# Performance work log

Hardware: AMD Instinct MI355X
Metric: run time of the kernel (lower is better)

Reference implementation:

```python
import jax, jax.numpy as jnp
import numpy as np

B, T, D, K = 8, 2048, 384, 64

def setup_inputs() -> dict:
    key = jax.random.key(0)
    k1, k2, k3, k4 = jax.random.split(key, 4)
    x = jax.random.normal(k1, (B, T, D), dtype=jnp.float32)
    # torch nn.Linear default init scale ~ 1/sqrt(fan_in); use scaled normals
    Wq = jax.random.normal(k2, (D, K), dtype=jnp.float32) / np.sqrt(D)
    Wk = jax.random.normal(k3, (D, K), dtype=jnp.float32) / np.sqrt(D)
    Wv = jax.random.normal(k4, (D, D), dtype=jnp.float32) / np.sqrt(D)
    return {"x": x, "Wq": Wq, "Wk": Wk, "Wv": Wv}

def reference(x, Wq, Wk, Wv):
    # x: (B,T,D)
    q = jnp.einsum('btd,dk->btk', x, Wq)      # (B,T,K)
    k = jnp.einsum('btd,dk->btk', x, Wk)      # (B,T,K)
    v = jnp.einsum('btd,de->bte', x, Wv)      # (B,T,D)
    scores = jnp.einsum('bqk,bsk->bqs', q, k) / jnp.sqrt(jnp.float32(K))  # (B,T,T)
    causal = jnp.tril(jnp.ones((T, T), dtype=bool))
    scores = jnp.where(causal, scores, -jnp.inf)
    weights = jax.nn.softmax(scores, axis=-1)
    out = jnp.einsum('bqs,bse->bqe', weights, v)  # (B,T,D)
    return out
```

## Files before the change

kernel.cpp:

```cpp
#include <hip/hip_runtime.h>

#define TT 2048
#define DD 384

typedef float f32x4 __attribute__((ext_vector_type(4)));
typedef float f32x16 __attribute__((ext_vector_type(16)));
typedef short s16x8 __attribute__((ext_vector_type(8)));
typedef short s16x2 __attribute__((ext_vector_type(2)));
typedef unsigned int u32x4 __attribute__((ext_vector_type(4)));

typedef __attribute__((address_space(3))) unsigned char* as3p;
typedef const __attribute__((address_space(1))) unsigned char* as1p;
#define GLLDS(gsrc, ldst) __builtin_amdgcn_global_load_lds((as1p)(gsrc), (as3p)(ldst), 16, 0, 0)

static __device__ __forceinline__ unsigned short f2bf(float f) {
    unsigned int u = __builtin_bit_cast(unsigned int, f);
    u = (u + 0x7fffu + ((u >> 16) & 1u)) >> 16;
    return (unsigned short)u;
}
static __device__ __forceinline__ unsigned int pk2(float a, float b) {
#if __has_builtin(__builtin_amdgcn_cvt_pk_bf16_f32)
    s16x2 t = __builtin_amdgcn_cvt_pk_bf16_f32(a, b);
    return __builtin_bit_cast(unsigned int, t);
#else
    unsigned int ua = __builtin_bit_cast(unsigned int, a);
    unsigned int ub = __builtin_bit_cast(unsigned int, b);
    ua = (ua + 0x7fffu + ((ua >> 16) & 1u)) >> 16;
    ub = (ub + 0x7fffu + ((ub >> 16) & 1u)) & 0xffff0000u;
    return ua | ub;
#endif
}

__global__ __launch_bounds__(256, 2) void qkv_gemm(
    const float* __restrict__ x, const float* __restrict__ Wq,
    const float* __restrict__ Wk, const float* __restrict__ Wv,
    unsigned short* __restrict__ qo, unsigned short* __restrict__ ko,
    unsigned short* __restrict__ vto)
{
    __shared__ __align__(16) unsigned short lds[16384];
    const int tid = threadIdx.x;
    const int l   = tid & 63;
    const int w   = tid >> 6;
    const int si  = l & 15;
    const int qq  = l >> 4;
    const int m0  = blockIdx.x * 128;
    const int nb  = blockIdx.y;
    const int wr  = w >> 1, wc = w & 1;

    const int bn = tid & 127;
    const int bk = (tid >> 7) * 16;
    const float* wsrc; int ldw;
    if (nb == 0) { wsrc = (bn < 64) ? (Wq + bn) : (Wk + (bn - 64)); ldw = 64; }
    else         { wsrc = Wv + (nb - 1) * 128 + bn;                 ldw = 384; }

    f32x4 acc[4][4];
    #pragma unroll
    for (int rt = 0; rt < 4; ++rt)
        #pragma unroll
        for (int ct = 0; ct < 4; ++ct) acc[rt][ct] = (f32x4){0.f, 0.f, 0.f, 0.f};

    for (int kt = 0; kt < 12; ++kt) {
        const int k0 = kt * 32;
        #pragma unroll
        for (int i = 0; i < 2; ++i) {
            const int u = tid + 256 * i, r = u >> 2, c = u & 3;
            const float* xp = x + (size_t)(m0 + r) * DD + k0 + c * 8;
            f32x4 x0 = *(const f32x4*)xp;
            f32x4 x1 = *(const f32x4*)(xp + 4);
            s16x8 av;
            av[0] = (short)f2bf(x0[0]); av[1] = (short)f2bf(x0[1]);
            av[2] = (short)f2bf(x0[2]); av[3] = (short)f2bf(x0[3]);
            av[4] = (short)f2bf(x1[0]); av[5] = (short)f2bf(x1[1]);
            av[6] = (short)f2bf(x1[2]); av[7] = (short)f2bf(x1[3]);
            *(s16x8*)&lds[r * 32 + ((c ^ (r & 3)) * 8)] = av;
        }
        {
            float t[16];
            #pragma unroll
            for (int j = 0; j < 16; ++j) t[j] = wsrc[(size_t)(k0 + bk + j) * ldw];
            #pragma unroll
            for (int jj = 0; jj < 2; ++jj) {
                s16x8 bv;
                #pragma unroll
                for (int j = 0; j < 8; ++j) bv[j] = (short)f2bf(t[jj * 8 + j]);
                const int ch = (tid >> 7) * 2 + jj;
                *(s16x8*)&lds[4096 + bn * 32 + ((ch ^ (bn & 3)) * 8)] = bv;
            }
        }
        __syncthreads();

        s16x8 af[4], bf[4];
        #pragma unroll
        for (int rt = 0; rt < 4; ++rt) {
            const int row = wr * 64 + rt * 16 + si;
            af[rt] = *(const s16x8*)&lds[row * 32 + ((qq ^ (row & 3)) * 8)];
        }
        #pragma unroll
        for (int ct = 0; ct < 4; ++ct) {
            const int col = wc * 64 + ct * 16 + si;
            bf[ct] = *(const s16x8*)&lds[4096 + col * 32 + ((qq ^ (col & 3)) * 8)];
        }
        #pragma unroll
        for (int rt = 0; rt < 4; ++rt)
            #pragma unroll
            for (int ct = 0; ct < 4; ++ct)
                acc[rt][ct] = __builtin_amdgcn_mfma_f32_16x16x32_bf16(af[rt], bf[ct], acc[rt][ct], 0, 0, 0);
        __syncthreads();
    }

    if (nb == 0) {
        if (wc == 0) {
            #pragma unroll
            for (int rt = 0; rt < 4; ++rt)
                #pragma unroll
                for (int ct = 0; ct < 4; ++ct)
                    #pragma unroll
                    for (int r = 0; r < 4; ++r) {
                        const int m = m0 + wr * 64 + rt * 16 + qq * 4 + r;
                        qo[(size_t)m * 64 + ct * 16 + si] = f2bf(acc[rt][ct][r] * 0.125f);
                    }
        } else {
            #pragma unroll
            for (int rt = 0; rt < 4; ++rt)
                #pragma unroll
                for (int ct = 0; ct < 4; ++ct)
                    #pragma unroll
                    for (int r = 0; r < 4; ++r) {
                        const int m = m0 + wr * 64 + rt * 16 + qq * 4 + r;
                        const int col = ct * 16 + si;
                        ko[(size_t)m * 64 + (((col >> 3) ^ (m & 7)) * 8) + (col & 7)] = f2bf(acc[rt][ct][r]);
                    }
        }
    } else {
        #pragma unroll
        for (int rt = 0; rt < 4; ++rt)
            #pragma unroll
            for (int ct = 0; ct < 4; ++ct)
                #pragma unroll
                for (int r = 0; r < 4; ++r) {
                    const int m = wr * 64 + rt * 16 + qq * 4 + r;
                    const int n = wc * 64 + ct * 16 + si;
                    lds[n * 128 + (((m >> 3) ^ (n & 7)) * 8) + (m & 7)] = f2bf(acc[rt][ct][r]);
                }
        __syncthreads();
        const int bbat = m0 >> 11, t0 = m0 & 2047;
        #pragma unroll
        for (int i = 0; i < 8; ++i) {
            const int u = tid + 256 * i, n = u >> 4, mc = u & 15;
            s16x8 v = *(const s16x8*)&lds[n * 128 + ((mc ^ (n & 7)) * 8)];
            *(s16x8*)&vto[((size_t)bbat * DD + ((nb - 1) * 128 + n)) * TT
                          + t0 + (mc >> 3) * 64 + (((mc & 7) ^ (n & 7)) * 8)] = v;
        }
    }
}

__global__ __launch_bounds__(1024, 4) void attn(
    const unsigned short* __restrict__ qg, const unsigned short* __restrict__ kg,
    const unsigned short* __restrict__ vg, float* __restrict__ out)
{
    __shared__ __align__(16) unsigned short lds[40960];

    const int tid = threadIdx.x;
    const int l   = tid & 63;
    const int w   = tid >> 6;
    const int q4  = w >> 2;
    const int qb  = w & 3;
    const int lo  = l & 31;
    const int hi  = l >> 5;
    const int h   = q4 >> 1;
    const int ct  = q4 & 1;

    const int g  = blockIdx.x;
    const int bb = g & 7;
    const int eq = (g >> 3) & 3;
    const int j  = 15 - (g >> 5);
    const int q0 = j * 128;
    const int e0 = eq * 96;
    const int qrow = q0 + qb * 32 + lo;

    s16x8 qf[4];
    {
        const unsigned short* qp = qg + ((size_t)bb * TT + qrow) * 64;
        #pragma unroll
        for (int st = 0; st < 4; ++st) qf[st] = *(const s16x8*)(qp + st * 16 + hi * 8);
    }

    f32x16 o[3];
    #pragma unroll
    for (int et = 0; et < 3; ++et)
        #pragma unroll
        for (int r = 0; r < 16; ++r) o[et][r] = 0.f;
    float lp = 0.f;

    const unsigned short* kbase = kg + (size_t)bb * TT * 64;
    const unsigned short* vbase = vg + ((size_t)bb * DD + e0) * TT;

    const unsigned short* kS = kbase + w * 512 + l * 8;
    const int chA = w,      pA = chA / 12, rrA = (chA % 12) * 8;
    const int chB = 16 + w, pB = chB / 12, rrB = (chB % 12) * 8;
    const unsigned short* vSA = vbase + ((size_t)(rrA + (l >> 3))) * TT + pA * 64 + (l & 7) * 8;
    const unsigned short* vSB = vbase + ((size_t)(rrB + (l >> 3))) * TT + pB * 64 + (l & 7) * 8;

    #define STAGE(IT, BUF)                                                   \
    {                                                                        \
        unsigned short* kl = &lds[(BUF) * 8192];                             \
        GLLDS(kS + (size_t)(IT) * 8192, &kl[w * 512]);                       \
        unsigned short* vl = &lds[16384 + (BUF) * 12288];                    \
        GLLDS(vSA + (IT) * 128, &vl[chA * 512]);                             \
        if (w < 8) GLLDS(vSB + (IT) * 128, &vl[chB * 512]);                  \
    }

    STAGE(0, 0);

    for (int it = 0; it <= j; ++it) {
        const int buf = it & 1;
        __syncthreads();

        if (it < j) STAGE(it + 1, 1 - buf);

        const unsigned short* Ks = &lds[buf * 8192 + h * 4096];
        const unsigned short* Vs = &lds[16384 + buf * 12288 + h * 6144];

        const int sq = it * 128 + q4 * 32;
        if (sq <= q0 + qb * 32 + 31) {
            const bool mb = (sq + 31 > q0 + qb * 32);
            f32x16 sa;
            #pragma unroll
            for (int r = 0; r < 16; ++r) sa[r] = 0.f;
            #pragma unroll
            for (int st = 0; st < 4; ++st) {
                s16x8 kf = *(const s16x8*)&Ks[(ct * 32 + lo) * 64 + (((st * 2 + hi) ^ (lo & 7)) * 8)];
                sa = __builtin_amdgcn_mfma_f32_32x32x16_bf16(kf, qf[st], sa, 0, 0, 0);
            }
            float pv[16];
            #pragma unroll
            for (int r = 0; r < 16; ++r) {
                float e = __expf(sa[r]);
                if (mb) {
                    const int srow = sq + (r & 3) + 8 * (r >> 2) + 4 * hi;
                    if (srow > qrow) e = 0.f;
                }
                pv[r] = e;
                lp += e;
            }
            unsigned int d0 = pk2(pv[0], pv[1]),   d1 = pk2(pv[2], pv[3]);
            unsigned int d2 = pk2(pv[4], pv[5]),   d3 = pk2(pv[6], pv[7]);
            unsigned int d4 = pk2(pv[8], pv[9]),   d5 = pk2(pv[10], pv[11]);
            unsigned int d6 = pk2(pv[12], pv[13]), d7 = pk2(pv[14], pv[15]);
            unsigned int sA0 = hi ? d0 : d2, sA1 = hi ? d1 : d3;
            unsigned int rA0 = (unsigned int)__shfl_xor((int)sA0, 32);
            unsigned int rA1 = (unsigned int)__shfl_xor((int)sA1, 32);
            u32x4 fa0 = hi ? (u32x4){rA0, rA1, d2, d3} : (u32x4){d0, d1, rA0, rA1};
            unsigned int sB0 = hi ? d4 : d6, sB1 = hi ? d5 : d7;
            unsigned int rB0 = (unsigned int)__shfl_xor((int)sB0, 32);
            unsigned int rB1 = (unsigned int)__shfl_xor((int)sB1, 32);
            u32x4 fa1 = hi ? (u32x4){rB0, rB1, d6, d7} : (u32x4){d4, d5, rB0, rB1};
            s16x8 a0 = __builtin_bit_cast(s16x8, fa0);
            s16x8 a1 = __builtin_bit_cast(s16x8, fa1);
            #pragma unroll
            for (int et = 0; et < 3; ++et) {
                const int el = et * 32 + lo;
                s16x8 v0 = *(const s16x8*)&Vs[el * 64 + (((ct * 4 + hi) ^ (el & 7)) * 8)];
                o[et] = __builtin_amdgcn_mfma_f32_32x32x16_bf16(a0, v0, o[et], 0, 0, 0);
                s16x8 v1 = *(const s16x8*)&Vs[el * 64 + (((ct * 4 + 2 + hi) ^ (el & 7)) * 8)];
                o[et] = __builtin_amdgcn_mfma_f32_32x32x16_bf16(a1, v1, o[et], 0, 0, 0);
            }
        }
    }
    __syncthreads();

    float* stL = (float*)lds;
    float* fb  = (float*)lds + 512;
    lp += __shfl_xor(lp, 32);
    if (hi == 0) stL[q4 * 128 + qb * 32 + lo] = lp;
    __syncthreads();

    #pragma unroll
    for (int ph = 0; ph < 2; ++ph) {
        if (q4 != 0 && (qb >> 1) == ph) {
            const int slot = (q4 - 1) * 64 + (qb & 1) * 32;
            #pragma unroll
            for (int r = 0; r < 16; ++r) {
                const int rloc = (r & 3) + 8 * (r >> 2) + 4 * hi;
                #pragma unroll
                for (int et = 0; et < 3; ++et)
                    fb[(slot + rloc) * 96 + et * 32 + lo] = o[et][r];
            }
        }
        __syncthreads();
        if (q4 == 0 && (qb >> 1) == ph) {
            const int slot = (qb & 1) * 32;
            #pragma unroll
            for (int r = 0; r < 16; ++r) {
                const int rloc = (r & 3) + 8 * (r >> 2) + 4 * hi;
                const int rr = qb * 32 + rloc;
                const float linv = 1.f / (stL[rr] + stL[128 + rr] + stL[256 + rr] + stL[384 + rr]);
                float* op = out + ((size_t)bb * TT + q0 + rr) * DD + e0;
                #pragma unroll
                for (int et = 0; et < 3; ++et)
                    op[et * 32 + lo] = (o[et][r]
                        + fb[(0 * 64 + slot + rloc) * 96 + et * 32 + lo]
                        + fb[(1 * 64 + slot + rloc) * 96 + et * 32 + lo]
                        + fb[(2 * 64 + slot + rloc) * 96 + et * 32 + lo]) * linv;
            }
        }
        __syncthreads();
    }
    #undef STAGE
}

extern "C" void kernel_launch(void* const* d_in, const int* in_sizes, int n_in,
                              void* d_out, int out_size, void* d_ws, size_t ws_size,
                              hipStream_t stream)
{
    const float* x  = (const float*)d_in[0];
    const float* Wq = (const float*)d_in[1];
    const float* Wk = (const float*)d_in[2];
    const float* Wv = (const float*)d_in[3];

    unsigned short* qws  = (unsigned short*)d_ws;
    unsigned short* kws  = (unsigned short*)((char*)d_ws + ((size_t)2 << 20));
    unsigned short* vtws = (unsigned short*)((char*)d_ws + ((size_t)4 << 20));

    qkv_gemm<<<dim3(128, 4), dim3(256), 0, stream>>>(x, Wq, Wk, Wv, qws, kws, vtws);
    attn<<<dim3(512), dim3(1024), 0, stream>>>(qws, kws, vtws, (float*)d_out);
}
```

Baseline: 150.4 us.

## Split fused attention into separate QK/softmax and PV kernels via materialized P

```diff
diff --git a/kernel.cpp b/kernel.cpp
--- a/kernel.cpp
+++ b/kernel.cpp
@@ -154,30 +154,29 @@
     }
 }
 
-__global__ __launch_bounds__(1024, 4) void attn(
+__global__ __launch_bounds__(256, 4) void qk_pass(
     const unsigned short* __restrict__ qg, const unsigned short* __restrict__ kg,
-    const unsigned short* __restrict__ vg, float* __restrict__ out)
+    unsigned short* __restrict__ Pws, float* __restrict__ lpart)
 {
-    __shared__ __align__(16) unsigned short lds[40960];
-
+    __shared__ __align__(16) unsigned short kl[8192];
     const int tid = threadIdx.x;
     const int l   = tid & 63;
     const int w   = tid >> 6;
-    const int q4  = w >> 2;
-    const int qb  = w & 3;
     const int lo  = l & 31;
     const int hi  = l >> 5;
-    const int h   = q4 >> 1;
-    const int ct  = q4 & 1;
-
-    const int g  = blockIdx.x;
-    const int bb = g & 7;
-    const int eq = (g >> 3) & 3;
-    const int j  = 15 - (g >> 5);
-    const int q0 = j * 128;
-    const int e0 = eq * 96;
-    const int qrow = q0 + qb * 32 + lo;
-
+    const int t   = blockIdx.x;
+    const int bb  = blockIdx.y;
+
+    int j = 0, acc = 0;
+    while (acc + j + 1 <= t) { acc += j + 1; ++j; }
+    const int it = t - acc;
+
+    const unsigned short* kS = kg + (size_t)bb * TT * 64 + (size_t)it * 8192;
+    #pragma unroll
+    for (int c = 0; c < 4; ++c)
+        GLLDS(kS + (w * 4 + c) * 512 + l * 8, &kl[(w * 4 + c) * 512]);
+
+    const int qrow = j * 128 + w * 32 + lo;
     s16x8 qf[4];
     {
         const unsigned short* qp = qg + ((size_t)bb * TT + qrow) * 64;
@@ -185,81 +184,120 @@
         for (int st = 0; st < 4; ++st) qf[st] = *(const s16x8*)(qp + st * 16 + hi * 8);
     }
 
-    f32x16 o[3];
-    #pragma unroll
-    for (int et = 0; et < 3; ++et)
+    __syncthreads();
+
+    float lp = 0.f;
+    const bool onD = (it == j);
+    unsigned short* pt = Pws + (size_t)(bb * 136 + t) * 16384;
+    const int nsq = onD ? (w + 1) : 4;
+    for (int sq = 0; sq < nsq; ++sq) {
+        f32x16 sa;
+        #pragma unroll
+        for (int r = 0; r < 16; ++r) sa[r] = 0.f;
+        #pragma unroll
+        for (int st = 0; st < 4; ++st) {
+            s16x8 kf = *(const s16x8*)&kl[(sq * 32 + lo) * 64 + (((st * 2 + hi) ^ (lo & 7)) * 8)];
+            sa = __builtin_amdgcn_mfma_f32_32x32x16_bf16(kf, qf[st], sa, 0, 0, 0);
+        }
+        const bool mb = onD && (sq == w);
+        float pv[16];
+        #pragma unroll
+        for (int r = 0; r < 16; ++r) {
+            float e = __expf(sa[r]);
+            if (mb) {
+                const int srow = it * 128 + sq * 32 + (r & 3) + 8 * (r >> 2) + 4 * hi;
+                if (srow > qrow) e = 0.f;
+            }
+            pv[r] = e;
+            lp += e;
+        }
+        unsigned int d0 = pk2(pv[0], pv[1]),   d1 = pk2(pv[2], pv[3]);
+        unsigned int d2 = pk2(pv[4], pv[5]),   d3 = pk2(pv[6], pv[7]);
+        unsigned int d4 = pk2(pv[8], pv[9]),   d5 = pk2(pv[10], pv[11]);
+        unsigned int d6 = pk2(pv[12], pv[13]), d7 = pk2(pv[14], pv[15]);
+        unsigned int sA0 = hi ? d0 : d2, sA1 = hi ? d1 : d3;
+        unsigned int rA0 = (unsigned int)__shfl_xor((int)sA0, 32);
+        unsigned int rA1 = (unsigned int)__shfl_xor((int)sA1, 32);
+        u32x4 fa0 = hi ? (u32x4){rA0, rA1, d2, d3} : (u32x4){d0, d1, rA0, rA1};
+        unsigned int sB0 = hi ? d4 : d6, sB1 = hi ? d5 : d7;
+        unsigned int rB0 = (unsigned int)__shfl_xor((int)sB0, 32);
+        unsigned int rB1 = (unsigned int)__shfl_xor((int)sB1, 32);
+        u32x4 fa1 = hi ? (u32x4){rB0, rB1, d6, d7} : (u32x4){d4, d5, rB0, rB1};
+        *(s16x8*)(pt + (w * 4 + sq) * 1024 + l * 8)       = __builtin_bit_cast(s16x8, fa0);
+        *(s16x8*)(pt + (w * 4 + sq) * 1024 + 512 + l * 8) = __builtin_bit_cast(s16x8, fa1);
+    }
+    lp += __shfl_xor(lp, 32);
+    if (hi == 0)
+        lpart[((size_t)bb * 16 + it) * 2048 + (size_t)j * 128 + w * 32 + lo] = lp;
+}
+
+__global__ __launch_bounds__(512, 4) void pv_pass(
+    const unsigned short* __restrict__ Pws, const unsigned short* __restrict__ vg,
+    const float* __restrict__ lpart, float* __restrict__ out)
+{
+    __shared__ __align__(16) unsigned short vl[32768];
+    __shared__ float linv[128];
+    const int tid = threadIdx.x;
+    const int l   = tid & 63;
+    const int w   = tid >> 6;
+    const int qb  = w >> 1;
+    const int ew  = w & 1;
+    const int lo  = l & 31;
+    const int hi  = l >> 5;
+
+    const int g  = blockIdx.x;
+    const int m  = g >> 1, p = g & 1;
+    const int jj = m / 12;
+    const int j  = p ? jj : 15 - jj;
+    const int combo = (m % 12) * 2 + p;
+    const int bb = combo & 7;
+    const int eb = combo >> 3;
+
+    const unsigned short* ptile = Pws + (size_t)(bb * 136 + j * (j + 1) / 2) * 16384;
+    const unsigned short* vbase = vg + ((size_t)bb * DD + eb * 128) * TT;
+
+    if (tid < 128) {
+        float s = 0.f;
+        for (int it = 0; it <= j; ++it)
+            s += lpart[((size_t)bb * 16 + it) * 2048 + (size_t)j * 128 + tid];
+        linv[tid] = 1.f / s;
+    }
+
+    const unsigned short* vS[4];
+    #pragma unroll
+    for (int c = 0; c < 4; ++c) {
+        const int ch = w * 4 + c, ph = ch >> 4, rg = ch & 15;
+        vS[c] = vbase + (size_t)(rg * 8 + (l >> 3)) * TT + ph * 64 + (l & 7) * 8;
+    }
+    #define VSTAGE(IT, BUF)                                                     \
+    {                                                                           \
+        _Pragma("unroll")                                                       \
+        for (int c = 0; c < 4; ++c)                                             \
+            GLLDS(vS[c] + (size_t)(IT) * 128, &vl[(BUF) * 16384 + (w * 4 + c) * 512]); \
+    }
+
+    f32x16 o[2];
+    #pragma unroll
+    for (int et = 0; et < 2; ++et)
         #pragma unroll
         for (int r = 0; r < 16; ++r) o[et][r] = 0.f;
-    float lp = 0.f;
-
-    const unsigned short* kbase = kg + (size_t)bb * TT * 64;
-    const unsigned short* vbase = vg + ((size_t)bb * DD + e0) * TT;
-
-    const unsigned short* kS = kbase + w * 512 + l * 8;
-    const int chA = w,      pA = chA / 12, rrA = (chA % 12) * 8;
-    const int chB = 16 + w, pB = chB / 12, rrB = (chB % 12) * 8;
-    const unsigned short* vSA = vbase + ((size_t)(rrA + (l >> 3))) * TT + pA * 64 + (l & 7) * 8;
-    const unsigned short* vSB = vbase + ((size_t)(rrB + (l >> 3))) * TT + pB * 64 + (l & 7) * 8;
-
-    #define STAGE(IT, BUF)                                                   \
-    {                                                                        \
-        unsigned short* kl = &lds[(BUF) * 8192];                             \
-        GLLDS(kS + (size_t)(IT) * 8192, &kl[w * 512]);                       \
-        unsigned short* vl = &lds[16384 + (BUF) * 12288];                    \
-        GLLDS(vSA + (IT) * 128, &vl[chA * 512]);                             \
-        if (w < 8) GLLDS(vSB + (IT) * 128, &vl[chB * 512]);                  \
-    }
-
-    STAGE(0, 0);
-
+
+    VSTAGE(0, 0);
     for (int it = 0; it <= j; ++it) {
         const int buf = it & 1;
         __syncthreads();
-
-        if (it < j) STAGE(it + 1, 1 - buf);
-
-        const unsigned short* Ks = &lds[buf * 8192 + h * 4096];
-        const unsigned short* Vs = &lds[16384 + buf * 12288 + h * 6144];
-
-        const int sq = it * 128 + q4 * 32;
-        if (sq <= q0 + qb * 32 + 31) {
-            const bool mb = (sq + 31 > q0 + qb * 32);
-            f32x16 sa;
-            #pragma unroll
-            for (int r = 0; r < 16; ++r) sa[r] = 0.f;
-            #pragma unroll
-            for (int st = 0; st < 4; ++st) {
-                s16x8 kf = *(const s16x8*)&Ks[(ct * 32 + lo) * 64 + (((st * 2 + hi) ^ (lo & 7)) * 8)];
-                sa = __builtin_amdgcn_mfma_f32_32x32x16_bf16(kf, qf[st], sa, 0, 0, 0);
-            }
-            float pv[16];
-            #pragma unroll
-            for (int r = 0; r < 16; ++r) {
-                float e = __expf(sa[r]);
-                if (mb) {
-                    const int srow = sq + (r & 3) + 8 * (r >> 2) + 4 * hi;
-                    if (srow > qrow) e = 0.f;
-                }
-                pv[r] = e;
-                lp += e;
-            }
-            unsigned int d0 = pk2(pv[0], pv[1]),   d1 = pk2(pv[2], pv[3]);
-            unsigned int d2 = pk2(pv[4], pv[5]),   d3 = pk2(pv[6], pv[7]);
-            unsigned int d4 = pk2(pv[8], pv[9]),   d5 = pk2(pv[10], pv[11]);
-            unsigned int d6 = pk2(pv[12], pv[13]), d7 = pk2(pv[14], pv[15]);
-            unsigned int sA0 = hi ? d0 : d2, sA1 = hi ? d1 : d3;
-            unsigned int rA0 = (unsigned int)__shfl_xor((int)sA0, 32);
-            unsigned int rA1 = (unsigned int)__shfl_xor((int)sA1, 32);
-            u32x4 fa0 = hi ? (u32x4){rA0, rA1, d2, d3} : (u32x4){d0, d1, rA0, rA1};
-            unsigned int sB0 = hi ? d4 : d6, sB1 = hi ? d5 : d7;
-            unsigned int rB0 = (unsigned int)__shfl_xor((int)sB0, 32);
-            unsigned int rB1 = (unsigned int)__shfl_xor((int)sB1, 32);
-            u32x4 fa1 = hi ? (u32x4){rB0, rB1, d6, d7} : (u32x4){d4, d5, rB0, rB1};
-            s16x8 a0 = __builtin_bit_cast(s16x8, fa0);
-            s16x8 a1 = __builtin_bit_cast(s16x8, fa1);
-            #pragma unroll
-            for (int et = 0; et < 3; ++et) {
-                const int el = et * 32 + lo;
+        if (it < j) VSTAGE(it + 1, 1 - buf);
+
+        const unsigned short* pfr = ptile + (size_t)it * 16384 + qb * 4096;
+        const int nsq = (it == j) ? (qb + 1) : 4;
+        for (int sq = 0; sq < nsq; ++sq) {
+            s16x8 a0 = *(const s16x8*)(pfr + sq * 1024 + l * 8);
+            s16x8 a1 = *(const s16x8*)(pfr + sq * 1024 + 512 + l * 8);
+            const int h = sq >> 1, ct = sq & 1;
+            const unsigned short* Vs = &vl[buf * 16384 + h * 8192];
+            #pragma unroll
+            for (int et = 0; et < 2; ++et) {
+                const int el = ew * 64 + et * 32 + lo;
                 s16x8 v0 = *(const s16x8*)&Vs[el * 64 + (((ct * 4 + hi) ^ (el & 7)) * 8)];
                 o[et] = __builtin_amdgcn_mfma_f32_32x32x16_bf16(a0, v0, o[et], 0, 0, 0);
                 s16x8 v1 = *(const s16x8*)&Vs[el * 64 + (((ct * 4 + 2 + hi) ^ (el & 7)) * 8)];
@@ -267,46 +305,17 @@
             }
         }
     }
-    __syncthreads();
-
-    float* stL = (float*)lds;
-    float* fb  = (float*)lds + 512;
-    lp += __shfl_xor(lp, 32);
-    if (hi == 0) stL[q4 * 128 + qb * 32 + lo] = lp;
-    __syncthreads();
-
-    #pragma unroll
-    for (int ph = 0; ph < 2; ++ph) {
-        if (q4 != 0 && (qb >> 1) == ph) {
-            const int slot = (q4 - 1) * 64 + (qb & 1) * 32;
-            #pragma unroll
-            for (int r = 0; r < 16; ++r) {
-                const int rloc = (r & 3) + 8 * (r >> 2) + 4 * hi;
-                #pragma unroll
-                for (int et = 0; et < 3; ++et)
-                    fb[(slot + rloc) * 96 + et * 32 + lo] = o[et][r];
-            }
-        }
-        __syncthreads();
-        if (q4 == 0 && (qb >> 1) == ph) {
-            const int slot = (qb & 1) * 32;
-            #pragma unroll
-            for (int r = 0; r < 16; ++r) {
-                const int rloc = (r & 3) + 8 * (r >> 2) + 4 * hi;
-                const int rr = qb * 32 + rloc;
-                const float linv = 1.f / (stL[rr] + stL[128 + rr] + stL[256 + rr] + stL[384 + rr]);
-                float* op = out + ((size_t)bb * TT + q0 + rr) * DD + e0;
-                #pragma unroll
-                for (int et = 0; et < 3; ++et)
-                    op[et * 32 + lo] = (o[et][r]
-                        + fb[(0 * 64 + slot + rloc) * 96 + et * 32 + lo]
-                        + fb[(1 * 64 + slot + rloc) * 96 + et * 32 + lo]
-                        + fb[(2 * 64 + slot + rloc) * 96 + et * 32 + lo]) * linv;
-            }
-        }
-        __syncthreads();
-    }
-    #undef STAGE
+    #undef VSTAGE
+
+    #pragma unroll
+    for (int et = 0; et < 2; ++et)
+        #pragma unroll
+        for (int r = 0; r < 16; ++r) {
+            const int rloc = (r & 3) + 8 * (r >> 2) + 4 * hi;
+            const int row  = qb * 32 + rloc;
+            out[((size_t)bb * TT + j * 128 + row) * DD + eb * 128 + ew * 64 + et * 32 + lo]
+                = o[et][r] * linv[row];
+        }
 }
 
 extern "C" void kernel_launch(void* const* d_in, const int* in_sizes, int n_in,
@@ -321,7 +330,10 @@
     unsigned short* qws  = (unsigned short*)d_ws;
     unsigned short* kws  = (unsigned short*)((char*)d_ws + ((size_t)2 << 20));
     unsigned short* vtws = (unsigned short*)((char*)d_ws + ((size_t)4 << 20));
+    unsigned short* Pws  = (unsigned short*)((char*)d_ws + ((size_t)16 << 20));
+    float*          lpart = (float*)((char*)d_ws + ((size_t)16 << 20) + (size_t)8 * 136 * 32768);
 
     qkv_gemm<<<dim3(128, 4), dim3(256), 0, stream>>>(x, Wq, Wk, Wv, qws, kws, vtws);
-    attn<<<dim3(512), dim3(1024), 0, stream>>>(qws, kws, vtws, (float*)d_out);
-}
+    qk_pass<<<dim3(136, 8), dim3(256), 0, stream>>>(qws, kws, Pws, lpart);
+    pv_pass<<<dim3(384), dim3(512), 0, stream>>>(Pws, vtws, lpart, (float*)d_out);
+}
```

After: 150.2 us. No clear change (-0.1%).

## Restructure attention into smaller blocks with software-pipelined PV via LDS-staged probabilities

Applied to the files above, without the earlier changes.

```diff
diff --git a/kernel.cpp b/kernel.cpp
--- a/kernel.cpp
+++ b/kernel.cpp
@@ -154,7 +154,7 @@
     }
 }
 
-__global__ __launch_bounds__(1024, 4) void attn(
+__global__ __launch_bounds__(256, 2) void attn(
     const unsigned short* __restrict__ qg, const unsigned short* __restrict__ kg,
     const unsigned short* __restrict__ vg, float* __restrict__ out)
 {
@@ -163,20 +163,19 @@
     const int tid = threadIdx.x;
     const int l   = tid & 63;
     const int w   = tid >> 6;
-    const int q4  = w >> 2;
-    const int qb  = w & 3;
+    const int qh  = w >> 1;
+    const int eg  = w & 1;
     const int lo  = l & 31;
     const int hi  = l >> 5;
-    const int h   = q4 >> 1;
-    const int ct  = q4 & 1;
-
-    const int g  = blockIdx.x;
-    const int bb = g & 7;
-    const int eq = (g >> 3) & 3;
-    const int j  = 15 - (g >> 5);
-    const int q0 = j * 128;
-    const int e0 = eq * 96;
-    const int qrow = q0 + qb * 32 + lo;
+
+    const int g    = blockIdx.x;
+    const int bb   = g & 7;
+    const int rest = g >> 3;
+    const int eh   = rest % 3;
+    const int q2   = 31 - rest / 3;
+    const int q0   = q2 * 64;
+    const int e0   = eh * 128;
+    const int qrow = q0 + qh * 32 + lo;
 
     s16x8 qf[4];
     {
@@ -185,9 +184,9 @@
         for (int st = 0; st < 4; ++st) qf[st] = *(const s16x8*)(qp + st * 16 + hi * 8);
     }
 
-    f32x16 o[3];
+    f32x16 o[2];
     #pragma unroll
-    for (int et = 0; et < 3; ++et)
+    for (int et = 0; et < 2; ++et)
         #pragma unroll
         for (int r = 0; r < 16; ++r) o[et][r] = 0.f;
     float lp = 0.f;
@@ -195,49 +194,63 @@
     const unsigned short* kbase = kg + (size_t)bb * TT * 64;
     const unsigned short* vbase = vg + ((size_t)bb * DD + e0) * TT;
 
-    const unsigned short* kS = kbase + w * 512 + l * 8;
-    const int chA = w,      pA = chA / 12, rrA = (chA % 12) * 8;
-    const int chB = 16 + w, pB = chB / 12, rrB = (chB % 12) * 8;
-    const unsigned short* vSA = vbase + ((size_t)(rrA + (l >> 3))) * TT + pA * 64 + (l & 7) * 8;
-    const unsigned short* vSB = vbase + ((size_t)(rrB + (l >> 3))) * TT + pB * 64 + (l & 7) * 8;
-
-    #define STAGE(IT, BUF)                                                   \
-    {                                                                        \
-        unsigned short* kl = &lds[(BUF) * 8192];                             \
-        GLLDS(kS + (size_t)(IT) * 8192, &kl[w * 512]);                       \
-        unsigned short* vl = &lds[16384 + (BUF) * 12288];                    \
-        GLLDS(vSA + (IT) * 128, &vl[chA * 512]);                             \
-        if (w < 8) GLLDS(vSB + (IT) * 128, &vl[chB * 512]);                  \
-    }
-
-    STAGE(0, 0);
-
-    for (int it = 0; it <= j; ++it) {
-        const int buf = it & 1;
+    #define STAGE(IT, KB, VB)                                                              \
+    {                                                                                      \
+        GLLDS(kbase + (size_t)(IT) * 4096 + (2 * w) * 512 + l * 8,                         \
+              &lds[(KB) * 4096 + (2 * w) * 512]);                                          \
+        GLLDS(kbase + (size_t)(IT) * 4096 + (2 * w + 1) * 512 + l * 8,                     \
+              &lds[(KB) * 4096 + (2 * w + 1) * 512]);                                      \
+        _Pragma("unroll")                                                                  \
+        for (int c3 = 0; c3 < 4; ++c3) {                                                   \
+            const int rg = 4 * w + c3;                                                     \
+            GLLDS(vbase + (size_t)(rg * 8 + (l >> 3)) * TT + (IT) * 64 + (l & 7) * 8,      \
+                  &lds[8192 + (VB) * 8192 + rg * 512]);                                    \
+        }                                                                                  \
+    }
+
+    #define PVSTEP(VB, PB)                                                                 \
+    {                                                                                      \
+        _Pragma("unroll")                                                                  \
+        for (int ss = 0; ss < 2; ++ss) {                                                   \
+            s16x8 a0 = *(const s16x8*)&lds[32768 + (PB) * 4096 + (qh * 2 + ss) * 1024 + l * 8];       \
+            s16x8 a1 = *(const s16x8*)&lds[32768 + (PB) * 4096 + (qh * 2 + ss) * 1024 + 512 + l * 8]; \
+            _Pragma("unroll")                                                              \
+            for (int et = 0; et < 2; ++et) {                                               \
+                const int el = eg * 64 + et * 32 + lo;                                     \
+                const int vbse = 8192 + (VB) * 8192 + el * 64;                             \
+                s16x8 v0 = *(const s16x8*)&lds[vbse + (((ss * 4 + hi) ^ (el & 7)) * 8)];   \
+                o[et] = __builtin_amdgcn_mfma_f32_32x32x16_bf16(a0, v0, o[et], 0, 0, 0);   \
+                s16x8 v1 = *(const s16x8*)&lds[vbse + (((ss * 4 + 2 + hi) ^ (el & 7)) * 8)]; \
+                o[et] = __builtin_amdgcn_mfma_f32_32x32x16_bf16(a1, v1, o[et], 0, 0, 0);   \
+            }                                                                              \
+        }                                                                                  \
+    }
+
+    STAGE(0, 0, 0);
+
+    int vi = 0, vn = 1;
+    for (int it = 0; it <= q2; ++it) {
+        const int kb = it & 1;
         __syncthreads();
 
-        if (it < j) STAGE(it + 1, 1 - buf);
-
-        const unsigned short* Ks = &lds[buf * 8192 + h * 4096];
-        const unsigned short* Vs = &lds[16384 + buf * 12288 + h * 6144];
-
-        const int sq = it * 128 + q4 * 32;
-        if (sq <= q0 + qb * 32 + 31) {
-            const bool mb = (sq + 31 > q0 + qb * 32);
+        if (it < q2) STAGE(it + 1, 1 - kb, vn);
+
+        {
             f32x16 sa;
             #pragma unroll
             for (int r = 0; r < 16; ++r) sa[r] = 0.f;
             #pragma unroll
             for (int st = 0; st < 4; ++st) {
-                s16x8 kf = *(const s16x8*)&Ks[(ct * 32 + lo) * 64 + (((st * 2 + hi) ^ (lo & 7)) * 8)];
+                s16x8 kf = *(const s16x8*)&lds[kb * 4096 + (eg * 32 + lo) * 64 + (((st * 2 + hi) ^ (lo & 7)) * 8)];
                 sa = __builtin_amdgcn_mfma_f32_32x32x16_bf16(kf, qf[st], sa, 0, 0, 0);
             }
+            const bool mb = (it == q2);
             float pv[16];
             #pragma unroll
             for (int r = 0; r < 16; ++r) {
                 float e = __expf(sa[r]);
                 if (mb) {
-                    const int srow = sq + (r & 3) + 8 * (r >> 2) + 4 * hi;
+                    const int srow = it * 64 + eg * 32 + (r & 3) + 8 * (r >> 2) + 4 * hi;
                     if (srow > qrow) e = 0.f;
                 }
                 pv[r] = e;
@@ -255,58 +268,40 @@
             unsigned int rB0 = (unsigned int)__shfl_xor((int)sB0, 32);
             unsigned int rB1 = (unsigned int)__shfl_xor((int)sB1, 32);
             u32x4 fa1 = hi ? (u32x4){rB0, rB1, d6, d7} : (u32x4){d4, d5, rB0, rB1};
-            s16x8 a0 = __builtin_bit_cast(s16x8, fa0);
-            s16x8 a1 = __builtin_bit_cast(s16x8, fa1);
-            #pragma unroll
-            for (int et = 0; et < 3; ++et) {
-                const int el = et * 32 + lo;
-                s16x8 v0 = *(const s16x8*)&Vs[el * 64 + (((ct * 4 + hi) ^ (el & 7)) * 8)];
-                o[et] = __builtin_amdgcn_mfma_f32_32x32x16_bf16(a0, v0, o[et], 0, 0, 0);
-                s16x8 v1 = *(const s16x8*)&Vs[el * 64 + (((ct * 4 + 2 + hi) ^ (el & 7)) * 8)];
-                o[et] = __builtin_amdgcn_mfma_f32_32x32x16_bf16(a1, v1, o[et], 0, 0, 0);
-            }
-        }
+            *(s16x8*)&lds[32768 + kb * 4096 + (qh * 2 + eg) * 1024 + l * 8]       = __builtin_bit_cast(s16x8, fa0);
+            *(s16x8*)&lds[32768 + kb * 4096 + (qh * 2 + eg) * 1024 + 512 + l * 8] = __builtin_bit_cast(s16x8, fa1);
+        }
+
+        if (it > 0) {
+            const int vp = (vi == 0) ? 2 : vi - 1;
+            PVSTEP(vp, 1 - kb);
+        }
+
+        vi = vn; vn = (vn == 2) ? 0 : vn + 1;
     }
     __syncthreads();
-
-    float* stL = (float*)lds;
-    float* fb  = (float*)lds + 512;
+    {
+        const int vlast = (vi == 0) ? 2 : vi - 1;
+        PVSTEP(vlast, q2 & 1);
+    }
+    __syncthreads();
+
+    float* stL = (float*)&lds[32768];
     lp += __shfl_xor(lp, 32);
-    if (hi == 0) stL[q4 * 128 + qb * 32 + lo] = lp;
+    if (hi == 0) stL[(qh * 2 + eg) * 32 + lo] = lp;
     __syncthreads();
 
     #pragma unroll
-    for (int ph = 0; ph < 2; ++ph) {
-        if (q4 != 0 && (qb >> 1) == ph) {
-            const int slot = (q4 - 1) * 64 + (qb & 1) * 32;
-            #pragma unroll
-            for (int r = 0; r < 16; ++r) {
-                const int rloc = (r & 3) + 8 * (r >> 2) + 4 * hi;
-                #pragma unroll
-                for (int et = 0; et < 3; ++et)
-                    fb[(slot + rloc) * 96 + et * 32 + lo] = o[et][r];
-            }
-        }
-        __syncthreads();
-        if (q4 == 0 && (qb >> 1) == ph) {
-            const int slot = (qb & 1) * 32;
-            #pragma unroll
-            for (int r = 0; r < 16; ++r) {
-                const int rloc = (r & 3) + 8 * (r >> 2) + 4 * hi;
-                const int rr = qb * 32 + rloc;
-                const float linv = 1.f / (stL[rr] + stL[128 + rr] + stL[256 + rr] + stL[384 + rr]);
-                float* op = out + ((size_t)bb * TT + q0 + rr) * DD + e0;
-                #pragma unroll
-                for (int et = 0; et < 3; ++et)
-                    op[et * 32 + lo] = (o[et][r]
-                        + fb[(0 * 64 + slot + rloc) * 96 + et * 32 + lo]
-                        + fb[(1 * 64 + slot + rloc) * 96 + et * 32 + lo]
-                        + fb[(2 * 64 + slot + rloc) * 96 + et * 32 + lo]) * linv;
-            }
-        }
-        __syncthreads();
-    }
+    for (int et = 0; et < 2; ++et)
+        #pragma unroll
+        for (int r = 0; r < 16; ++r) {
+            const int rloc = (r & 3) + 8 * (r >> 2) + 4 * hi;
+            const float linv = 1.f / (stL[qh * 64 + rloc] + stL[qh * 64 + 32 + rloc]);
+            out[((size_t)bb * TT + q0 + qh * 32 + rloc) * DD + e0 + eg * 64 + et * 32 + lo]
+                = o[et][r] * linv;
+        }
     #undef STAGE
+    #undef PVSTEP
 }
 
 extern "C" void kernel_launch(void* const* d_in, const int* in_sizes, int n_in,
@@ -323,5 +318,5 @@
     unsigned short* vtws = (unsigned short*)((char*)d_ws + ((size_t)4 << 20));
 
     qkv_gemm<<<dim3(128, 4), dim3(256), 0, stream>>>(x, Wq, Wk, Wv, qws, kws, vtws);
-    attn<<<dim3(512), dim3(1024), 0, stream>>>(qws, kws, vtws, (float*)d_out);
-}
+    attn<<<dim3(768), dim3(256), 0, stream>>>(qws, kws, vtws, (float*)d_out);
+}
```

Result: faster. 140.3 us (-6.7%).
